# Optimization experiments

Hardware: AMD Instinct MI355X
Metric: run time of the kernel (lower is better)

Reference implementation:

```python
import jax, jax.numpy as jnp
import numpy as np

B = 32768
D_A, D_V, D_T = 512, 512, 768
D_KW, D_CTX, D_SPK = 256, 256, 128
H = 512
IN_A = D_V + D_T + D_KW + D_CTX + D_SPK  # 1920 = visual + other_dim (text+hidden+speaker)
IN_V = D_A + D_T + D_KW + D_CTX + D_SPK  # 1920


def _linear_params(key, din, dout):
    kw, kb = jax.random.split(key)
    bound = 1.0 / np.sqrt(din)
    W = jax.random.uniform(kw, (din, dout), jnp.float32, -bound, bound)
    b = jax.random.uniform(kb, (dout,), jnp.float32, -bound, bound)
    return W, b


def setup_inputs() -> dict:
    key = jax.random.key(0)
    ks = jax.random.split(key, 16)
    inp = {
        'audio': jax.random.normal(ks[0], (B, D_A), jnp.float32),
        'visual': jax.random.normal(ks[1], (B, D_V), jnp.float32),
        'text': jax.random.normal(ks[2], (B, D_T), jnp.float32),
        'keywords': jax.random.normal(ks[3], (B, D_KW), jnp.float32),
        'context': jax.random.normal(ks[4], (B, D_CTX), jnp.float32),
        'speaker_embed': jax.random.normal(ks[5], (B, D_SPK), jnp.float32),
    }
    # Masks restricted to dimensionally-consistent patterns: [0,1,1] or [1,0,1]
    r = jax.random.randint(ks[6], (B,), 0, 2)
    inp['modality_masks'] = jnp.stack([r, 1 - r, jnp.ones_like(r)], axis=1).astype(jnp.int32)
    # audio_imagination MLP params
    inp['aW1'], inp['ab1'] = _linear_params(ks[7], IN_A, H)
    inp['aW2'], inp['ab2'] = _linear_params(ks[8], H, H)
    inp['aW3'], inp['ab3'] = _linear_params(ks[9], H, D_A)
    # visual_imagination MLP params
    inp['vW1'], inp['vb1'] = _linear_params(ks[10], IN_V, H)
    inp['vW2'], inp['vb2'] = _linear_params(ks[11], H, H)
    inp['vW3'], inp['vb3'] = _linear_params(ks[12], H, D_V)
    return inp


def _mlp(x, W1, b1, W2, b2, W3, b3):
    h = jax.nn.relu(x @ W1 + b1)  # dropout is eval-mode identity
    h = jax.nn.relu(h @ W2 + b2)
    return h @ W3 + b3


def reference(audio, visual, text, keywords, context, speaker_embed, modality_masks,
              aW1, ab1, aW2, ab2, aW3, ab3,
              vW1, vb1, vW2, vb2, vW3, vb3):
    m = modality_masks.astype(audio.dtype)
    common = jnp.concatenate([keywords, context, speaker_embed], axis=-1)  # [B, 640]
    in_a = jnp.concatenate([visual, text, common], axis=-1)  # [B, IN_A]
    in_v = jnp.concatenate([audio, text, common], axis=-1)   # [B, IN_V]
    # Rows where the modality is present (mask==1) were omitted in the original
    # ragged stacking; here they are zeroed to keep a fixed [B, D] output.
    recon_audio = _mlp(in_a, aW1, ab1, aW2, ab2, aW3, ab3) * (1.0 - m[:, 0:1])
    recon_visual = _mlp(in_v, vW1, vb1, vW2, vb2, vW3, vb3) * (1.0 - m[:, 1:2])
    return recon_audio, recon_visual
```

## Files before the change

kernel.cpp:

```cpp
#include <hip/hip_runtime.h>
#include <stdint.h>

typedef __bf16 bf16;
typedef __bf16 bf16x8 __attribute__((ext_vector_type(8)));
typedef float  f32x4  __attribute__((ext_vector_type(4)));

#define NROWS 32768
#define HID   512

__device__ __forceinline__ void gload_lds16(const void* g, void* l) {
  __builtin_amdgcn_global_load_lds(
      (const __attribute__((address_space(1))) void*)g,
      (__attribute__((address_space(3))) void*)l, 16, 0, 0);
}

__global__ void prep_transpose(const float* __restrict__ W, bf16* __restrict__ WT,
                               int K, int N) {
  __shared__ float t[32][33];
  int k0 = blockIdx.x * 32, n0 = blockIdx.y * 32;
  int tx = threadIdx.x, ty = threadIdx.y;
#pragma unroll
  for (int p = 0; p < 4; ++p)
    t[ty + p * 8][tx] = W[(size_t)(k0 + ty + p * 8) * N + n0 + tx];
  __syncthreads();
#pragma unroll
  for (int p = 0; p < 4; ++p) {
    int n = n0 + ty + p * 8;
    int k = k0 + tx;
    int ks = (k & ~63) | (((((k >> 3) & 7) ^ (n & 7))) << 3) | (k & 7);
    WT[(size_t)n * K + ks] = (bf16)t[tx][ty + p * 8];
  }
}

__global__ void count_rows(const int* __restrict__ masks, int* __restrict__ bcnt) {
  int i = blockIdx.x * 256 + threadIdx.x;
  int lane = threadIdx.x & 63, wv = threadIdx.x >> 6;
  unsigned long long vA = __ballot(masks[i * 3] == 0);
  __shared__ int c[4];
  if (lane == 0) c[wv] = __popcll(vA);
  __syncthreads();
  if (threadIdx.x == 0) bcnt[blockIdx.x] = c[0] + c[1] + c[2] + c[3];
}

__global__ void scan_blocks(const int* __restrict__ bcnt, int* __restrict__ baseA,
                            int* __restrict__ counts) {
  __shared__ int s[128];
  s[threadIdx.x] = bcnt[threadIdx.x];
  __syncthreads();
  if (threadIdx.x == 0) {
    int run = 0;
    for (int i = 0; i < 128; ++i) { int v = s[i]; s[i] = run; run += v; }
    counts[0] = run; counts[1] = NROWS - run;
  }
  __syncthreads();
  baseA[threadIdx.x] = s[threadIdx.x];
}

__global__ void write_idx(const int* __restrict__ masks, const int* __restrict__ baseA,
                          int* __restrict__ idxA, int* __restrict__ idxV) {
  int b = blockIdx.x, t = threadIdx.x, i = b * 256 + t;
  int lane = t & 63, wv = t >> 6;
  int r = masks[i * 3];
  unsigned long long vA = __ballot(r == 0);
  __shared__ int wc[4];
  if (lane == 0) wc[wv] = __popcll(vA);
  __syncthreads();
  int wA = 0;
#pragma unroll
  for (int w = 0; w < 4; ++w) if (w < wv) wA += wc[w];
  unsigned long long ltmask = (lane == 63) ? (~0ULL >> 1) : ((1ULL << lane) - 1);
  int posA = __popcll(vA & ltmask);
  int bA = baseA[b];
  if (r == 0) idxA[bA + wA + posA] = i;
  else        idxV[(256 * b - bA) + (64 * wv - wA) + (lane - posA)] = i;
}

template <int LAYER>
__global__ __launch_bounds__(256, 2) void mlp_gemm(
    const float* __restrict__ audio, const float* __restrict__ visual,
    const float* __restrict__ text,  const float* __restrict__ kwd,
    const float* __restrict__ ctx,   const float* __restrict__ spk,
    const bf16*  __restrict__ hin,
    const bf16*  __restrict__ WTa,   const bf16* __restrict__ WTv,
    const float* __restrict__ ba,    const float* __restrict__ bv,
    const int*   __restrict__ counts,
    const int*   __restrict__ idxA,  const int* __restrict__ idxV,
    bf16* __restrict__ hout, float* __restrict__ out) {
  constexpr int K = (LAYER == 1) ? 1920 : 512;
  constexpr int NT = K / 64;
  const int mlp = blockIdx.z;
  const int cnt = counts[mlp];
  const int m0 = blockIdx.x * 128;
  if (m0 >= cnt) return;
  const int n0 = blockIdx.y * 128;
  const bf16*  WT   = mlp ? WTv : WTa;
  const float* bias = mlp ? bv : ba;
  const int*   idx  = mlp ? idxV : idxA;

  __shared__ __attribute__((aligned(16))) bf16 sA[128 * 64];
  __shared__ __attribute__((aligned(16))) bf16 sB[128 * 64];

  const int t = threadIdx.x;
  const int lane = t & 63;
  const int wave = t >> 6;
  const int wm = (wave >> 1) * 64;
  const int wn = (wave & 1) * 64;

  int gidx[4];
  if constexpr (LAYER == 1) {
#pragma unroll
    for (int rep = 0; rep < 4; ++rep) {
      int row = (t + rep * 256) >> 3;
      int i = m0 + row;
      if (i >= cnt) i = cnt - 1;
      gidx[rep] = idx[i];
    }
  }

  auto B_ISSUE = [&](int k0) {
#pragma unroll
    for (int j = 0; j < 4; ++j) {
      int sbase = (wave * 4 + j) * 64;
      int slot = sbase + lane;
      int row = slot >> 3, wc = slot & 7;
      gload_lds16(WT + (size_t)(n0 + row) * K + k0 + wc * 8, &sB[sbase * 8]);
    }
  };
  auto A_ISSUE_LDS = [&](int k0) {
#pragma unroll
    for (int j = 0; j < 4; ++j) {
      int sbase = (wave * 4 + j) * 64;
      int slot = sbase + lane;
      int row = slot >> 3, wc = slot & 7;
      gload_lds16(hin + ((size_t)mlp * NROWS + m0 + row) * HID + k0 + wc * 8,
                  &sA[sbase * 8]);
    }
  };

  const f32x4 fzero = {0.f, 0.f, 0.f, 0.f};
  f32x4 acc[4][4];
#pragma unroll
  for (int a = 0; a < 4; ++a)
#pragma unroll
    for (int b = 0; b < 4; ++b) acc[a][b] = fzero;

  for (int ti = 0; ti < NT; ++ti) {
    const int k0 = ti * 64;
    __syncthreads();
    B_ISSUE(k0);
    if constexpr (LAYER >= 2) {
      A_ISSUE_LDS(k0);
    } else {
      const float* seg; int soff, sstr;
      if (k0 < 512)       { seg = mlp ? audio : visual; soff = k0;        sstr = 512; }
      else if (k0 < 1280) { seg = text; soff = k0 - 512;  sstr = 768; }
      else if (k0 < 1536) { seg = kwd;  soff = k0 - 1280; sstr = 256; }
      else if (k0 < 1792) { seg = ctx;  soff = k0 - 1536; sstr = 256; }
      else                { seg = spk;  soff = k0 - 1792; sstr = 128; }
#pragma unroll
      for (int rep = 0; rep < 4; ++rep) {
        int slot = t + rep * 256;
        int row = slot >> 3, c = slot & 7;
        int wc = c ^ (row & 7);
        const float* src = seg + (size_t)gidx[rep] * sstr + soff + c * 8;
        f32x4 lo = *(const f32x4*)src;
        f32x4 hi = *(const f32x4*)(src + 4);
        bf16x8 v;
        v[0] = (bf16)lo[0]; v[1] = (bf16)lo[1]; v[2] = (bf16)lo[2]; v[3] = (bf16)lo[3];
        v[4] = (bf16)hi[0]; v[5] = (bf16)hi[1]; v[6] = (bf16)hi[2]; v[7] = (bf16)hi[3];
        *(bf16x8*)&sA[row * 64 + wc * 8] = v;
      }
    }
    __syncthreads();

    bf16x8 af[4][2], bfr[4][2];
#pragma unroll
    for (int mf = 0; mf < 4; ++mf)
#pragma unroll
      for (int kh = 0; kh < 2; ++kh) {
        int row = wm + mf * 16 + (lane & 15);
        int c = (lane >> 4) + kh * 4;
        af[mf][kh] = *(const bf16x8*)&sA[row * 64 + (c ^ (row & 7)) * 8];
      }
#pragma unroll
    for (int nf = 0; nf < 4; ++nf)
#pragma unroll
      for (int kh = 0; kh < 2; ++kh) {
        int row = wn + nf * 16 + (lane & 15);
        int c = (lane >> 4) + kh * 4;
        bfr[nf][kh] = *(const bf16x8*)&sB[row * 64 + (c ^ (row & 7)) * 8];
      }
#pragma unroll
    for (int mf = 0; mf < 4; ++mf)
#pragma unroll
      for (int nf = 0; nf < 4; ++nf)
#pragma unroll
        for (int kh = 0; kh < 2; ++kh)
          acc[mf][nf] = __builtin_amdgcn_mfma_f32_16x16x32_bf16(
              af[mf][kh], bfr[nf][kh], acc[mf][nf], 0, 0, 0);
  }

  const int r4 = (lane >> 4) * 4;
  const int cl = lane & 15;
#pragma unroll
  for (int mf = 0; mf < 4; ++mf) {
#pragma unroll
    for (int reg = 0; reg < 4; ++reg) {
      int lrow = wm + mf * 16 + r4 + reg;
      int grow = m0 + lrow;
      if (grow >= cnt) continue;
      if constexpr (LAYER < 3) {
#pragma unroll
        for (int nf = 0; nf < 4; ++nf) {
          int col = n0 + wn + nf * 16 + cl;
          float v = acc[mf][nf][reg] + bias[col];
          v = fmaxf(v, 0.f);
          int cs = (col & ~63) | (((((col >> 3) & 7) ^ (grow & 7))) << 3) | (col & 7);
          hout[((size_t)mlp * NROWS + grow) * HID + cs] = (bf16)v;
        }
      } else {
        int g = idx[grow];
#pragma unroll
        for (int nf = 0; nf < 4; ++nf) {
          int col = n0 + wn + nf * 16 + cl;
          float v = acc[mf][nf][reg] + bias[col];
          out[((size_t)mlp * NROWS + g) * 512 + col] = v;
          out[((size_t)(1 - mlp) * NROWS + g) * 512 + col] = 0.f;
        }
      }
    }
  }
}

extern "C" void kernel_launch(void* const* d_in, const int* in_sizes, int n_in,
                              void* d_out, int out_size, void* d_ws, size_t ws_size,
                              hipStream_t stream) {
  (void)in_sizes; (void)n_in; (void)out_size;
  const float* audio  = (const float*)d_in[0];
  const float* visual = (const float*)d_in[1];
  const float* text   = (const float*)d_in[2];
  const float* kwd    = (const float*)d_in[3];
  const float* ctx    = (const float*)d_in[4];
  const float* spk    = (const float*)d_in[5];
  const int*   masks  = (const int*)d_in[6];
  const float* aW1 = (const float*)d_in[7];  const float* ab1 = (const float*)d_in[8];
  const float* aW2 = (const float*)d_in[9];  const float* ab2 = (const float*)d_in[10];
  const float* aW3 = (const float*)d_in[11]; const float* ab3 = (const float*)d_in[12];
  const float* vW1 = (const float*)d_in[13]; const float* vb1 = (const float*)d_in[14];
  const float* vW2 = (const float*)d_in[15]; const float* vb2 = (const float*)d_in[16];
  const float* vW3 = (const float*)d_in[17]; const float* vb3 = (const float*)d_in[18];
  float* out = (float*)d_out;

  char* w = (char*)d_ws;
  int* counts = (int*)w;
  int* bcnt   = (int*)(w + 256);
  int* baseA  = (int*)(w + 1024);
  int* idxA = (int*)(w + 4096);
  int* idxV = idxA + 32768;
  bf16* aW1t = (bf16*)(w + 4096 + 262144);
  bf16* vW1t = aW1t + 983040;
  bf16* aW2t = vW1t + 983040;
  bf16* vW2t = aW2t + 262144;
  bf16* aW3t = vW2t + 262144;
  bf16* vW3t = aW3t + 262144;
  bf16* h1 = vW3t + 262144;
  bf16* h2 = h1 + (size_t)2 * NROWS * HID;
  (void)ws_size;

  count_rows<<<128, 256, 0, stream>>>(masks, bcnt);
  scan_blocks<<<1, 128, 0, stream>>>(bcnt, baseA, counts);
  write_idx<<<128, 256, 0, stream>>>(masks, baseA, idxA, idxV);

  dim3 tb(32, 8);
  prep_transpose<<<dim3(60, 16), tb, 0, stream>>>(aW1, aW1t, 1920, 512);
  prep_transpose<<<dim3(60, 16), tb, 0, stream>>>(vW1, vW1t, 1920, 512);
  prep_transpose<<<dim3(16, 16), tb, 0, stream>>>(aW2, aW2t, 512, 512);
  prep_transpose<<<dim3(16, 16), tb, 0, stream>>>(vW2, vW2t, 512, 512);
  prep_transpose<<<dim3(16, 16), tb, 0, stream>>>(aW3, aW3t, 512, 512);
  prep_transpose<<<dim3(16, 16), tb, 0, stream>>>(vW3, vW3t, 512, 512);

  dim3 gg(160, 4, 2);
  mlp_gemm<1><<<gg, 256, 0, stream>>>(audio, visual, text, kwd, ctx, spk, nullptr,
                                      aW1t, vW1t, ab1, vb1, counts, idxA, idxV, h1, nullptr);
  mlp_gemm<2><<<gg, 256, 0, stream>>>(audio, visual, text, kwd, ctx, spk, h1,
                                      aW2t, vW2t, ab2, vb2, counts, idxA, idxV, h2, nullptr);
  mlp_gemm<3><<<gg, 256, 0, stream>>>(audio, visual, text, kwd, ctx, spk, h2,
                                      aW3t, vW3t, ab3, vb3, counts, idxA, idxV, nullptr, out);
}
```

Baseline: 246.4 us.

## Restructure MLP GEMM with 3-stage LDS ring, direct weight register loads, 64x256 tiles

Reworks the gathered MLP GEMM kernels: tiles become 64 rows by 256 columns, with each wave owning 64 columns. Weight fragments are loaded straight from global memory into double-buffered registers instead of staging through LDS. Activations go through a 3-deep LDS ring filled with async global-to-LDS loads; layer 1 now stages raw fp32 rows and converts to bf16 on the LDS read. Explicit vmcnt waits, one barrier per k-step and MFMA priority boosts are meant to overlap loads with math. The block index is remapped, hidden buffers are padded to 17408 rows, and occupancy rises to 3 blocks per CU. The costs are more register pressure, a hand-tuned wait count that must match the issued loads, and possibly uncoalesced weight loads that rely on the cache.

```diff
diff --git a/kernel.cpp b/kernel.cpp
--- a/kernel.cpp
+++ b/kernel.cpp
@@ -7,6 +7,7 @@
 
 #define NROWS 32768
 #define HID   512
+#define PADM  17408
 
 __device__ __forceinline__ void gload_lds16(const void* g, void* l) {
   __builtin_amdgcn_global_load_lds(
@@ -16,20 +17,16 @@
 
 __global__ void prep_transpose(const float* __restrict__ W, bf16* __restrict__ WT,
                                int K, int N) {
-  __shared__ float t[32][33];
+  __shared__ float tt[32][33];
   int k0 = blockIdx.x * 32, n0 = blockIdx.y * 32;
   int tx = threadIdx.x, ty = threadIdx.y;
 #pragma unroll
   for (int p = 0; p < 4; ++p)
-    t[ty + p * 8][tx] = W[(size_t)(k0 + ty + p * 8) * N + n0 + tx];
-  __syncthreads();
-#pragma unroll
-  for (int p = 0; p < 4; ++p) {
-    int n = n0 + ty + p * 8;
-    int k = k0 + tx;
-    int ks = (k & ~63) | (((((k >> 3) & 7) ^ (n & 7))) << 3) | (k & 7);
-    WT[(size_t)n * K + ks] = (bf16)t[tx][ty + p * 8];
-  }
+    tt[ty + p * 8][tx] = W[(size_t)(k0 + ty + p * 8) * N + n0 + tx];
+  __syncthreads();
+#pragma unroll
+  for (int p = 0; p < 4; ++p)
+    WT[(size_t)(n0 + ty + p * 8) * K + k0 + tx] = (bf16)tt[tx][ty + p * 8];
 }
 
 __global__ void count_rows(const int* __restrict__ masks, int* __restrict__ bcnt) {
@@ -76,7 +73,7 @@
 }
 
 template <int LAYER>
-__global__ __launch_bounds__(256, 2) void mlp_gemm(
+__global__ __launch_bounds__(256, 3) void mlp_gemm(
     const float* __restrict__ audio, const float* __restrict__ visual,
     const float* __restrict__ text,  const float* __restrict__ kwd,
     const float* __restrict__ ctx,   const float* __restrict__ spk,
@@ -86,71 +83,46 @@
     const int*   __restrict__ counts,
     const int*   __restrict__ idxA,  const int* __restrict__ idxV,
     bf16* __restrict__ hout, float* __restrict__ out) {
-  constexpr int K = (LAYER == 1) ? 1920 : 512;
+  constexpr int K  = (LAYER == 1) ? 1920 : 512;
   constexpr int NT = K / 64;
+  constexpr int AL = (LAYER == 1) ? 4 : 2;
+  constexpr int AB = (LAYER == 1) ? 16384 : 8192;
   const int mlp = blockIdx.z;
   const int cnt = counts[mlp];
-  const int m0 = blockIdx.x * 128;
+  const int mb = (blockIdx.x & 7) * 34 + (blockIdx.x >> 3);
+  const int m0 = mb * 64;
   if (m0 >= cnt) return;
-  const int n0 = blockIdx.y * 128;
+  const int n0 = blockIdx.y * 256;
   const bf16*  WT   = mlp ? WTv : WTa;
   const float* bias = mlp ? bv : ba;
   const int*   idx  = mlp ? idxV : idxA;
 
-  __shared__ __attribute__((aligned(16))) bf16 sA[128 * 64];
-  __shared__ __attribute__((aligned(16))) bf16 sB[128 * 64];
+  __shared__ __attribute__((aligned(16))) char sA[3 * AB];
 
   const int t = threadIdx.x;
   const int lane = t & 63;
   const int wave = t >> 6;
-  const int wm = (wave >> 1) * 64;
-  const int wn = (wave & 1) * 64;
-
-  int gidx[4];
+  const int wn = wave * 64;
+  const int cl = lane & 15;
+  const int qw = lane >> 4;
+
+  int gidxA[AL];
   if constexpr (LAYER == 1) {
 #pragma unroll
-    for (int rep = 0; rep < 4; ++rep) {
-      int row = (t + rep * 256) >> 3;
+    for (int j = 0; j < AL; ++j) {
+      int slot = (j * 4 + wave) * 64 + lane;
+      int row = slot >> 4;
       int i = m0 + row;
       if (i >= cnt) i = cnt - 1;
-      gidx[rep] = idx[i];
+      gidxA[j] = idx[i];
     }
   }
 
-  auto B_ISSUE = [&](int k0) {
-#pragma unroll
-    for (int j = 0; j < 4; ++j) {
-      int sbase = (wave * 4 + j) * 64;
-      int slot = sbase + lane;
-      int row = slot >> 3, wc = slot & 7;
-      gload_lds16(WT + (size_t)(n0 + row) * K + k0 + wc * 8, &sB[sbase * 8]);
-    }
-  };
-  auto A_ISSUE_LDS = [&](int k0) {
-#pragma unroll
-    for (int j = 0; j < 4; ++j) {
-      int sbase = (wave * 4 + j) * 64;
-      int slot = sbase + lane;
-      int row = slot >> 3, wc = slot & 7;
-      gload_lds16(hin + ((size_t)mlp * NROWS + m0 + row) * HID + k0 + wc * 8,
-                  &sA[sbase * 8]);
-    }
-  };
-
-  const f32x4 fzero = {0.f, 0.f, 0.f, 0.f};
-  f32x4 acc[4][4];
-#pragma unroll
-  for (int a = 0; a < 4; ++a)
-#pragma unroll
-    for (int b = 0; b < 4; ++b) acc[a][b] = fzero;
-
-  for (int ti = 0; ti < NT; ++ti) {
+  auto STAGE_A = [&](int ti) {
+    const int ring = ti % 3;
     const int k0 = ti * 64;
-    __syncthreads();
-    B_ISSUE(k0);
-    if constexpr (LAYER >= 2) {
-      A_ISSUE_LDS(k0);
-    } else {
+    char* base = sA + ring * AB;
+    if constexpr (LAYER == 1) {
       const float* seg; int soff, sstr;
       if (k0 < 512)       { seg = mlp ? audio : visual; soff = k0;        sstr = 512; }
       else if (k0 < 1280) { seg = text; soff = k0 - 512;  sstr = 768; }
@@ -158,55 +130,116 @@
       else if (k0 < 1792) { seg = ctx;  soff = k0 - 1536; sstr = 256; }
       else                { seg = spk;  soff = k0 - 1792; sstr = 128; }
 #pragma unroll
-      for (int rep = 0; rep < 4; ++rep) {
-        int slot = t + rep * 256;
-        int row = slot >> 3, c = slot & 7;
-        int wc = c ^ (row & 7);
-        const float* src = seg + (size_t)gidx[rep] * sstr + soff + c * 8;
-        f32x4 lo = *(const f32x4*)src;
-        f32x4 hi = *(const f32x4*)(src + 4);
-        bf16x8 v;
-        v[0] = (bf16)lo[0]; v[1] = (bf16)lo[1]; v[2] = (bf16)lo[2]; v[3] = (bf16)lo[3];
-        v[4] = (bf16)hi[0]; v[5] = (bf16)hi[1]; v[6] = (bf16)hi[2]; v[7] = (bf16)hi[3];
-        *(bf16x8*)&sA[row * 64 + wc * 8] = v;
+      for (int j = 0; j < AL; ++j) {
+        int slot = (j * 4 + wave) * 64 + lane;
+        int row = slot >> 4, ch = slot & 15;
+        const float* src = seg + (size_t)gidxA[j] * sstr + soff + ((ch ^ (row & 15)) << 2);
+        gload_lds16(src, base + slot * 16);
+      }
+    } else {
+#pragma unroll
+      for (int j = 0; j < AL; ++j) {
+        int slot = (j * 4 + wave) * 64 + lane;
+        int row = slot >> 3, ch = slot & 7;
+        gload_lds16(hin + ((size_t)mlp * PADM + m0 + row) * HID + k0 + ch * 8,
+                    base + slot * 16);
       }
     }
-    __syncthreads();
-
-    bf16x8 af[4][2], bfr[4][2];
-#pragma unroll
-    for (int mf = 0; mf < 4; ++mf)
-#pragma unroll
-      for (int kh = 0; kh < 2; ++kh) {
-        int row = wm + mf * 16 + (lane & 15);
-        int c = (lane >> 4) + kh * 4;
-        af[mf][kh] = *(const bf16x8*)&sA[row * 64 + (c ^ (row & 7)) * 8];
-      }
+  };
+
+  bf16x8 brD[2][4][2];
+  auto LDB = [&](int ti, int buf) {
+    const bf16* p = WT + (size_t)(n0 + wn + cl) * K + ti * 64 + qw * 8;
 #pragma unroll
     for (int nf = 0; nf < 4; ++nf)
 #pragma unroll
-      for (int kh = 0; kh < 2; ++kh) {
-        int row = wn + nf * 16 + (lane & 15);
-        int c = (lane >> 4) + kh * 4;
-        bfr[nf][kh] = *(const bf16x8*)&sB[row * 64 + (c ^ (row & 7)) * 8];
-      }
-#pragma unroll
-    for (int mf = 0; mf < 4; ++mf)
-#pragma unroll
-      for (int nf = 0; nf < 4; ++nf)
-#pragma unroll
-        for (int kh = 0; kh < 2; ++kh)
+      for (int kh = 0; kh < 2; ++kh)
+        brD[buf][nf][kh] = *(const bf16x8*)(p + (size_t)nf * 16 * K + kh * 32);
+  };
+
+  const f32x4 fzero = {0.f, 0.f, 0.f, 0.f};
+  f32x4 acc[4][4];
+#pragma unroll
+  for (int a = 0; a < 4; ++a)
+#pragma unroll
+    for (int b = 0; b < 4; ++b) acc[a][b] = fzero;
+
+  STAGE_A(0);
+  LDB(0, 0);
+  STAGE_A(1);
+  LDB(1, 1);
+  if constexpr (LAYER == 1)
+    asm volatile("s_waitcnt vmcnt(12)" ::: "memory");
+  else
+    asm volatile("s_waitcnt vmcnt(10)" ::: "memory");
+  __builtin_amdgcn_sched_barrier(0);
+  __builtin_amdgcn_s_barrier();
+
+  for (int ti = 0; ti < NT; ++ti) {
+    const int ring = ti % 3;
+    const int cur = ti & 1;
+    const int tc = (ti + 2 < NT) ? (ti + 2) : (NT - 1);
+
+    STAGE_A(tc);
+
+    bf16x8 af[4][2];
+    if constexpr (LAYER == 1) {
+      const float* sA32 = (const float*)(sA + ring * AB);
+#pragma unroll
+      for (int mf = 0; mf < 4; ++mf)
+#pragma unroll
+        for (int kh = 0; kh < 2; ++kh) {
+          int row = mf * 16 + cl;
+          int c2 = 2 * (qw + kh * 4);
+          f32x4 a0 = *(const f32x4*)&sA32[row * 64 + ((c2 ^ (row & 15)) << 2)];
+          f32x4 a1 = *(const f32x4*)&sA32[row * 64 + (((c2 + 1) ^ (row & 15)) << 2)];
+          bf16x8 v;
+          v[0] = (bf16)a0[0]; v[1] = (bf16)a0[1]; v[2] = (bf16)a0[2]; v[3] = (bf16)a0[3];
+          v[4] = (bf16)a1[0]; v[5] = (bf16)a1[1]; v[6] = (bf16)a1[2]; v[7] = (bf16)a1[3];
+          af[mf][kh] = v;
+        }
+    } else {
+      const bf16* sAb = (const bf16*)(sA + ring * AB);
+#pragma unroll
+      for (int mf = 0; mf < 4; ++mf)
+#pragma unroll
+        for (int kh = 0; kh < 2; ++kh) {
+          int row = mf * 16 + cl;
+          int c = qw + kh * 4;
+          af[mf][kh] = *(const bf16x8*)&sAb[row * 64 + ((c ^ (row & 7)) << 3)];
+        }
+    }
+
+    asm volatile("s_waitcnt lgkmcnt(0)" ::: "memory");
+    __builtin_amdgcn_sched_barrier(0);
+    __builtin_amdgcn_s_setprio(1);
+#pragma unroll
+    for (int kh = 0; kh < 2; ++kh)
+#pragma unroll
+      for (int mf = 0; mf < 4; ++mf)
+#pragma unroll
+        for (int nf = 0; nf < 4; ++nf)
           acc[mf][nf] = __builtin_amdgcn_mfma_f32_16x16x32_bf16(
-              af[mf][kh], bfr[nf][kh], acc[mf][nf], 0, 0, 0);
+              af[mf][kh], brD[cur][nf][kh], acc[mf][nf], 0, 0, 0);
+    __builtin_amdgcn_s_setprio(0);
+    __builtin_amdgcn_sched_barrier(0);
+
+    LDB(tc, cur);
+
+    if constexpr (LAYER == 1)
+      asm volatile("s_waitcnt vmcnt(12)" ::: "memory");
+    else
+      asm volatile("s_waitcnt vmcnt(10)" ::: "memory");
+    __builtin_amdgcn_sched_barrier(0);
+    __builtin_amdgcn_s_barrier();
   }
-
-  const int r4 = (lane >> 4) * 4;
-  const int cl = lane & 15;
+  asm volatile("s_waitcnt vmcnt(0) lgkmcnt(0)" ::: "memory");
+
 #pragma unroll
   for (int mf = 0; mf < 4; ++mf) {
 #pragma unroll
     for (int reg = 0; reg < 4; ++reg) {
-      int lrow = wm + mf * 16 + r4 + reg;
+      int lrow = mf * 16 + qw * 4 + reg;
       int grow = m0 + lrow;
       if (grow >= cnt) continue;
       if constexpr (LAYER < 3) {
@@ -216,7 +249,7 @@
           float v = acc[mf][nf][reg] + bias[col];
           v = fmaxf(v, 0.f);
           int cs = (col & ~63) | (((((col >> 3) & 7) ^ (grow & 7))) << 3) | (col & 7);
-          hout[((size_t)mlp * NROWS + grow) * HID + cs] = (bf16)v;
+          hout[((size_t)mlp * PADM + grow) * HID + cs] = (bf16)v;
         }
       } else {
         int g = idx[grow];
@@ -264,7 +297,7 @@
   bf16* aW3t = vW2t + 262144;
   bf16* vW3t = aW3t + 262144;
   bf16* h1 = vW3t + 262144;
-  bf16* h2 = h1 + (size_t)2 * NROWS * HID;
+  bf16* h2 = h1 + (size_t)2 * PADM * HID;
   (void)ws_size;
 
   count_rows<<<128, 256, 0, stream>>>(masks, bcnt);
@@ -279,7 +312,7 @@
   prep_transpose<<<dim3(16, 16), tb, 0, stream>>>(aW3, aW3t, 512, 512);
   prep_transpose<<<dim3(16, 16), tb, 0, stream>>>(vW3, vW3t, 512, 512);
 
-  dim3 gg(160, 4, 2);
+  dim3 gg(272, 2, 2);
   mlp_gemm<1><<<gg, 256, 0, stream>>>(audio, visual, text, kwd, ctx, spk, nullptr,
                                       aW1t, vW1t, ab1, vb1, counts, idxA, idxV, h1, nullptr);
   mlp_gemm<2><<<gg, 256, 0, stream>>>(audio, visual, text, kwd, ctx, spk, h1,
```

Result: slower. 714.9 us (+190.1%).
